# Kernel optimization log

Hardware: AMD Instinct MI355X
Metric: run time of the kernel (lower is better)

The kernel has to match this reference:

```python
import jax, jax.numpy as jnp
import numpy as np


def setup_inputs() -> dict:
    key = jax.random.key(0)
    ks = jax.random.split(key, 8)
    N, T, U = 8, 200, 50
    E = D = J = 512
    V = 500
    s = lambda k, shape, fan_in: jax.random.normal(k, shape, jnp.float32) / np.sqrt(fan_in)
    return {
        "encoder_out": jax.random.normal(ks[0], (N, T, E), jnp.float32),
        "decoder_out": jax.random.normal(ks[1], (N, U, D), jnp.float32),
        "W_enc": s(ks[2], (J, E), E),
        "b_enc": jax.random.normal(ks[3], (J,), jnp.float32) * 0.01,
        "W_dec": s(ks[4], (J, D), D),
        "b_dec": jax.random.normal(ks[5], (J,), jnp.float32) * 0.01,
        "W_out": s(ks[6], (V, J), J),
        "b_out": jax.random.normal(ks[7], (V,), jnp.float32) * 0.01,
    }


def reference(encoder_out, decoder_out, W_enc, b_enc, W_dec, b_dec, W_out, b_out):
    # Project encoder (N,T,E)->(N,T,J) and decoder (N,U,D)->(N,U,J).
    enc_p = jnp.einsum("nte,je->ntj", encoder_out, W_enc) + b_enc
    dec_p = jnp.einsum("nud,jd->nuj", decoder_out, W_dec) + b_dec
    # Broadcast add -> (N,T,U,J), tanh, then linear to vocab -> (N,T,U,V).
    activations = jnp.tanh(enc_p[:, :, None, :] + dec_p[:, None, :, :])
    logits = jnp.einsum("ntuj,vj->ntuv", activations, W_out) + b_out
    return logits
```

## Files before the change

### kernel.cpp

```cpp
#include <hip/hip_runtime.h>
#include <hip/hip_bf16.h>
#include <stdint.h>

#define JD 512
#define VV 500

typedef short short8 __attribute__((ext_vector_type(8)));
typedef short short4v __attribute__((ext_vector_type(4)));
typedef float floatx4 __attribute__((ext_vector_type(4)));

__device__ inline short f2bf(float f) {
    uint32_t u = __float_as_uint(f);
    uint32_t r = (u + 0x7FFFu + ((u >> 16) & 1u)) >> 16;
    return (short)r;
}

__device__ inline float fast_tanh(float x) {
    float e = __builtin_amdgcn_exp2f(x * 2.8853900817779268f);
    return 1.0f - 2.0f * __builtin_amdgcn_rcpf(e + 1.0f);
}

__global__ __launch_bounds__(256) void prep_kernel(
    const float* __restrict__ Wout, short* __restrict__ WbF)
{
    int j = blockIdx.x * 256 + threadIdx.x;
    int l16 = j & 15;
    int q4  = (j >> 4) & 3;
    int in  = (j >> 6) & 7;
    int wn  = (j >> 9) & 3;
    int ks  = j >> 11;
    int v  = wn * 128 + in * 16 + l16;
    int k0 = ks * 32 + q4 * 8;
    short8 o;
    if (v < VV) {
        const float4* p = (const float4*)(Wout + (size_t)v * JD + k0);
        float4 a = p[0], b = p[1];
        o[0] = f2bf(a.x); o[1] = f2bf(a.y); o[2] = f2bf(a.z); o[3] = f2bf(a.w);
        o[4] = f2bf(b.x); o[5] = f2bf(b.y); o[6] = f2bf(b.z); o[7] = f2bf(b.w);
    } else {
        o = (short8){0,0,0,0,0,0,0,0};
    }
    *(short8*)(WbF + (size_t)j * 8) = o;
}

#define PST 72
__global__ __launch_bounds__(256) void proj_gemm(
    const float* __restrict__ enc, const float* __restrict__ dec,
    const float* __restrict__ Wenc, const float* __restrict__ Wdec,
    const float* __restrict__ b_enc, const float* __restrict__ b_dec,
    float* __restrict__ enc_p, float* __restrict__ dec_p)
{
    __shared__ short As[64 * PST];
    __shared__ short Bs[64 * PST];
    int bx = blockIdx.x, by = blockIdx.y;
    const float* A; const float* W; const float* bias; float* C; int M;
    if (bx < 25) { A = enc; W = Wenc; bias = b_enc; C = enc_p; M = 1600; }
    else { bx -= 25; A = dec; W = Wdec; bias = b_dec; C = dec_p; M = 400; }

    int tid = threadIdx.x;
    int lane = tid & 63, wv = tid >> 6;
    int wm = wv >> 1, wn = wv & 1;
    int l16 = lane & 15, q4 = lane >> 4;

    int ra = tid >> 2, ha = tid & 3;
    int m_st = bx * 64 + ra;
    bool valid = m_st < M;
    int wrow = by * 64 + ra;

    floatx4 acc[2][2];
    #pragma unroll
    for (int a = 0; a < 2; a++)
        #pragma unroll
        for (int b = 0; b < 2; b++) acc[a][b] = (floatx4){0.f, 0.f, 0.f, 0.f};

    for (int kk = 0; kk < 8; kk++) {
        int k0 = kk * 64;
        __syncthreads();
        {
            float4 v0 = make_float4(0.f, 0.f, 0.f, 0.f);
            float4 v1 = v0, v2 = v0, v3 = v0;
            if (valid) {
                const float4* p = (const float4*)(A + (size_t)m_st * JD + k0 + ha * 16);
                v0 = p[0]; v1 = p[1]; v2 = p[2]; v3 = p[3];
            }
            short8 o0, o1;
            o0[0] = f2bf(v0.x); o0[1] = f2bf(v0.y); o0[2] = f2bf(v0.z); o0[3] = f2bf(v0.w);
            o0[4] = f2bf(v1.x); o0[5] = f2bf(v1.y); o0[6] = f2bf(v1.z); o0[7] = f2bf(v1.w);
            o1[0] = f2bf(v2.x); o1[1] = f2bf(v2.y); o1[2] = f2bf(v2.z); o1[3] = f2bf(v2.w);
            o1[4] = f2bf(v3.x); o1[5] = f2bf(v3.y); o1[6] = f2bf(v3.z); o1[7] = f2bf(v3.w);
            *(short8*)&As[ra * PST + ha * 16]     = o0;
            *(short8*)&As[ra * PST + ha * 16 + 8] = o1;

            const float4* pb = (const float4*)(W + (size_t)wrow * JD + k0 + ha * 16);
            float4 w0 = pb[0], w1 = pb[1], w2 = pb[2], w3 = pb[3];
            short8 p0, p1;
            p0[0] = f2bf(w0.x); p0[1] = f2bf(w0.y); p0[2] = f2bf(w0.z); p0[3] = f2bf(w0.w);
            p0[4] = f2bf(w1.x); p0[5] = f2bf(w1.y); p0[6] = f2bf(w1.z); p0[7] = f2bf(w1.w);
            p1[0] = f2bf(w2.x); p1[1] = f2bf(w2.y); p1[2] = f2bf(w2.z); p1[3] = f2bf(w2.w);
            p1[4] = f2bf(w3.x); p1[5] = f2bf(w3.y); p1[6] = f2bf(w3.z); p1[7] = f2bf(w3.w);
            *(short8*)&Bs[ra * PST + ha * 16]     = p0;
            *(short8*)&Bs[ra * PST + ha * 16 + 8] = p1;
        }
        __syncthreads();
        #pragma unroll
        for (int h2 = 0; h2 < 2; h2++) {
            short8 af[2], bf[2];
            #pragma unroll
            for (int im = 0; im < 2; im++)
                af[im] = *(const short8*)&As[(wm * 32 + im * 16 + l16) * PST + h2 * 32 + q4 * 8];
            #pragma unroll
            for (int in = 0; in < 2; in++)
                bf[in] = *(const short8*)&Bs[(wn * 32 + in * 16 + l16) * PST + h2 * 32 + q4 * 8];
            #pragma unroll
            for (int im = 0; im < 2; im++)
                #pragma unroll
                for (int in = 0; in < 2; in++)
                    acc[im][in] = __builtin_amdgcn_mfma_f32_16x16x32_bf16(
                        af[im], bf[in], acc[im][in], 0, 0, 0);
        }
    }
    #pragma unroll
    for (int im = 0; im < 2; im++) {
        int mb = bx * 64 + wm * 32 + im * 16 + q4 * 4;
        #pragma unroll
        for (int rr = 0; rr < 4; rr++) {
            int m = mb + rr;
            if (m < M) {
                #pragma unroll
                for (int in = 0; in < 2; in++) {
                    int j = by * 64 + wn * 32 + in * 16 + l16;
                    C[(size_t)m * JD + j] = acc[im][in][rr] + bias[j];
                }
            }
        }
    }
}

#define AST 520
__global__ __launch_bounds__(512, 2) void fused_joiner(
    const float* __restrict__ enc_p, const float* __restrict__ dec_p,
    const short* __restrict__ WbF, const float* __restrict__ b_out,
    float* __restrict__ out)
{
    __shared__ short As[2][64 * AST];
    int tid = threadIdx.x;
    int mgrp = blockIdx.x;
    int vg   = blockIdx.y;
    int lane = tid & 63, wv = tid >> 6;
    int l16 = lane & 15, q4 = lane >> 4;

    int wn  = vg * 2 + (wv >> 2);
    int in0 = (wv & 3) * 2;
    int vb0 = wn * 128 + in0 * 16;

    short8 breg0[16], breg1[16];
    {
        const short* bp = WbF + q4 * 128 + l16 * 8 + (wn * 8 + in0) * 512;
        #pragma unroll
        for (int ks = 0; ks < 16; ks++) {
            breg0[ks] = *(const short8*)(bp + ks * 16384);
            breg1[ks] = *(const short8*)(bp + ks * 16384 + 512);
        }
    }

    float bo0, bo1;
    {
        int v0 = vb0 + l16, v1 = vb0 + 16 + l16;
        bo0 = (v0 < VV) ? b_out[v0] : 0.f;
        bo1 = (v1 < VV) ? b_out[v1] : 0.f;
    }

    int rsub = tid >> 7;
    int jf   = (tid & 127) * 4;

    for (int t = 0; t < 10; t++) {
        int m0 = (mgrp * 10 + t) * 64;
        short* buf = &As[t & 1][0];

        #pragma unroll 4
        for (int pass = 0; pass < 16; pass++) {
            int row = pass * 4 + rsub;
            int m = m0 + row;
            int er = m / 50;
            int n  = m / 10000;
            int dr = n * 50 + (m - er * 50);
            float4 e = *(const float4*)(enc_p + (size_t)er * JD + jf);
            float4 d = *(const float4*)(dec_p + (size_t)dr * JD + jf);
            short4v o;
            o[0] = f2bf(fast_tanh(e.x + d.x));
            o[1] = f2bf(fast_tanh(e.y + d.y));
            o[2] = f2bf(fast_tanh(e.z + d.z));
            o[3] = f2bf(fast_tanh(e.w + d.w));
            *(short4v*)&buf[row * AST + jf] = o;
        }
        __syncthreads();

        #pragma unroll
        for (int ms = 0; ms < 4; ms++) {
            int ab = (ms * 16 + l16) * AST + q4 * 8;
            floatx4 a0 = (floatx4){0.f, 0.f, 0.f, 0.f};
            floatx4 a1 = (floatx4){0.f, 0.f, 0.f, 0.f};
            #pragma unroll
            for (int ks = 0; ks < 16; ks++) {
                short8 af = *(const short8*)&buf[ab + ks * 32];
                a0 = __builtin_amdgcn_mfma_f32_16x16x32_bf16(af, breg0[ks], a0, 0, 0, 0);
                a1 = __builtin_amdgcn_mfma_f32_16x16x32_bf16(af, breg1[ks], a1, 0, 0, 0);
            }
            int v0 = vb0 + l16, v1 = vb0 + 16 + l16;
            #pragma unroll
            for (int rr = 0; rr < 4; rr++) {
                size_t orow = (size_t)(m0 + ms * 16 + q4 * 4 + rr) * VV;
                if (v0 < VV) out[orow + v0] = a0[rr] + bo0;
                if (v1 < VV) out[orow + v1] = a1[rr] + bo1;
            }
        }
    }
}

extern "C" void kernel_launch(void* const* d_in, const int* in_sizes, int n_in,
                              void* d_out, int out_size, void* d_ws, size_t ws_size,
                              hipStream_t stream)
{
    const float* enc   = (const float*)d_in[0];
    const float* dec   = (const float*)d_in[1];
    const float* Wenc  = (const float*)d_in[2];
    const float* b_enc = (const float*)d_in[3];
    const float* Wdec  = (const float*)d_in[4];
    const float* b_dec = (const float*)d_in[5];
    const float* Wout  = (const float*)d_in[6];
    const float* b_out = (const float*)d_in[7];
    float* out = (float*)d_out;

    char* ws = (char*)d_ws;
    short* WbF   = (short*)(ws + 0);
    float* enc_p = (float*)(ws + 524288);
    float* dec_p = (float*)(ws + 3801088);

    prep_kernel<<<128, 256, 0, stream>>>(Wout, WbF);
    proj_gemm<<<dim3(32, 8), 256, 0, stream>>>(enc, dec, Wenc, Wdec,
                                               b_enc, b_dec, enc_p, dec_p);
    fused_joiner<<<dim3(125, 2), 512, 0, stream>>>(enc_p, dec_p, WbF, b_out, out);
}
```

Before: 238.3 us.

## Software-pipeline tanh tile generation with MFMA and load full K in projection

The main joint kernel now builds the first activation tile up front. While the MFMAs run on the current tile, it prefetches enc/dec rows and writes the tanh'd bf16 values for the next tile into the other LDS buffer, so the tanh/load phase overlaps with matrix work. The projection GEMM now stages the whole K=512 extent of A and W into LDS in one pass, with one barrier instead of a per-chunk loop with two barriers. That raises LDS use to about 133KB per block, which may cut occupancy or exceed the LDS limit, and the prefetch adds register pressure.

Result: no change. 234.0 us (-1.8%).

```diff
diff --git a/kernel.cpp b/kernel.cpp
--- a/kernel.cpp
+++ b/kernel.cpp
@@ -43,15 +43,15 @@
     *(short8*)(WbF + (size_t)j * 8) = o;
 }
 
-#define PST 72
+#define QST 520
 __global__ __launch_bounds__(256) void proj_gemm(
     const float* __restrict__ enc, const float* __restrict__ dec,
     const float* __restrict__ Wenc, const float* __restrict__ Wdec,
     const float* __restrict__ b_enc, const float* __restrict__ b_dec,
     float* __restrict__ enc_p, float* __restrict__ dec_p)
 {
-    __shared__ short As[64 * PST];
-    __shared__ short Bs[64 * PST];
+    __shared__ short As[64 * QST];
+    __shared__ short Bs[64 * QST];
     int bx = blockIdx.x, by = blockIdx.y;
     const float* A; const float* W; const float* bias; float* C; int M;
     if (bx < 25) { A = enc; W = Wenc; bias = b_enc; C = enc_p; M = 1600; }
@@ -67,58 +67,57 @@
     bool valid = m_st < M;
     int wrow = by * 64 + ra;
 
+    #pragma unroll
+    for (int c = 0; c < 8; c++) {
+        int k0 = c * 64 + ha * 16;
+        float4 v0 = make_float4(0.f, 0.f, 0.f, 0.f);
+        float4 v1 = v0, v2 = v0, v3 = v0;
+        if (valid) {
+            const float4* p = (const float4*)(A + (size_t)m_st * JD + k0);
+            v0 = p[0]; v1 = p[1]; v2 = p[2]; v3 = p[3];
+        }
+        const float4* pb = (const float4*)(W + (size_t)wrow * JD + k0);
+        float4 w0 = pb[0], w1 = pb[1], w2 = pb[2], w3 = pb[3];
+        short8 o0, o1, p0, p1;
+        o0[0] = f2bf(v0.x); o0[1] = f2bf(v0.y); o0[2] = f2bf(v0.z); o0[3] = f2bf(v0.w);
+        o0[4] = f2bf(v1.x); o0[5] = f2bf(v1.y); o0[6] = f2bf(v1.z); o0[7] = f2bf(v1.w);
+        o1[0] = f2bf(v2.x); o1[1] = f2bf(v2.y); o1[2] = f2bf(v2.z); o1[3] = f2bf(v2.w);
+        o1[4] = f2bf(v3.x); o1[5] = f2bf(v3.y); o1[6] = f2bf(v3.z); o1[7] = f2bf(v3.w);
+        p0[0] = f2bf(w0.x); p0[1] = f2bf(w0.y); p0[2] = f2bf(w0.z); p0[3] = f2bf(w0.w);
+        p0[4] = f2bf(w1.x); p0[5] = f2bf(w1.y); p0[6] = f2bf(w1.z); p0[7] = f2bf(w1.w);
+        p1[0] = f2bf(w2.x); p1[1] = f2bf(w2.y); p1[2] = f2bf(w2.z); p1[3] = f2bf(w2.w);
+        p1[4] = f2bf(w3.x); p1[5] = f2bf(w3.y); p1[6] = f2bf(w3.z); p1[7] = f2bf(w3.w);
+        *(short8*)&As[ra * QST + k0]     = o0;
+        *(short8*)&As[ra * QST + k0 + 8] = o1;
+        *(short8*)&Bs[ra * QST + k0]     = p0;
+        *(short8*)&Bs[ra * QST + k0 + 8] = p1;
+    }
+    __syncthreads();
+
     floatx4 acc[2][2];
     #pragma unroll
     for (int a = 0; a < 2; a++)
         #pragma unroll
         for (int b = 0; b < 2; b++) acc[a][b] = (floatx4){0.f, 0.f, 0.f, 0.f};
 
-    for (int kk = 0; kk < 8; kk++) {
-        int k0 = kk * 64;
-        __syncthreads();
-        {
-            float4 v0 = make_float4(0.f, 0.f, 0.f, 0.f);
-            float4 v1 = v0, v2 = v0, v3 = v0;
-            if (valid) {
-                const float4* p = (const float4*)(A + (size_t)m_st * JD + k0 + ha * 16);
-                v0 = p[0]; v1 = p[1]; v2 = p[2]; v3 = p[3];
-            }
-            short8 o0, o1;
-            o0[0] = f2bf(v0.x); o0[1] = f2bf(v0.y); o0[2] = f2bf(v0.z); o0[3] = f2bf(v0.w);
-            o0[4] = f2bf(v1.x); o0[5] = f2bf(v1.y); o0[6] = f2bf(v1.z); o0[7] = f2bf(v1.w);
-            o1[0] = f2bf(v2.x); o1[1] = f2bf(v2.y); o1[2] = f2bf(v2.z); o1[3] = f2bf(v2.w);
-            o1[4] = f2bf(v3.x); o1[5] = f2bf(v3.y); o1[6] = f2bf(v3.z); o1[7] = f2bf(v3.w);
-            *(short8*)&As[ra * PST + ha * 16]     = o0;
-            *(short8*)&As[ra * PST + ha * 16 + 8] = o1;
-
-            const float4* pb = (const float4*)(W + (size_t)wrow * JD + k0 + ha * 16);
-            float4 w0 = pb[0], w1 = pb[1], w2 = pb[2], w3 = pb[3];
-            short8 p0, p1;
-            p0[0] = f2bf(w0.x); p0[1] = f2bf(w0.y); p0[2] = f2bf(w0.z); p0[3] = f2bf(w0.w);
-            p0[4] = f2bf(w1.x); p0[5] = f2bf(w1.y); p0[6] = f2bf(w1.z); p0[7] = f2bf(w1.w);
-            p1[0] = f2bf(w2.x); p1[1] = f2bf(w2.y); p1[2] = f2bf(w2.z); p1[3] = f2bf(w2.w);
-            p1[4] = f2bf(w3.x); p1[5] = f2bf(w3.y); p1[6] = f2bf(w3.z); p1[7] = f2bf(w3.w);
-            *(short8*)&Bs[ra * PST + ha * 16]     = p0;
-            *(short8*)&Bs[ra * PST + ha * 16 + 8] = p1;
-        }
-        __syncthreads();
-        #pragma unroll
-        for (int h2 = 0; h2 < 2; h2++) {
-            short8 af[2], bf[2];
-            #pragma unroll
-            for (int im = 0; im < 2; im++)
-                af[im] = *(const short8*)&As[(wm * 32 + im * 16 + l16) * PST + h2 * 32 + q4 * 8];
+    #pragma unroll
+    for (int ks = 0; ks < 16; ks++) {
+        int ko = ks * 32 + q4 * 8;
+        short8 af[2], bf[2];
+        #pragma unroll
+        for (int im = 0; im < 2; im++)
+            af[im] = *(const short8*)&As[(wm * 32 + im * 16 + l16) * QST + ko];
+        #pragma unroll
+        for (int in = 0; in < 2; in++)
+            bf[in] = *(const short8*)&Bs[(wn * 32 + in * 16 + l16) * QST + ko];
+        #pragma unroll
+        for (int im = 0; im < 2; im++)
             #pragma unroll
             for (int in = 0; in < 2; in++)
-                bf[in] = *(const short8*)&Bs[(wn * 32 + in * 16 + l16) * PST + h2 * 32 + q4 * 8];
-            #pragma unroll
-            for (int im = 0; im < 2; im++)
-                #pragma unroll
-                for (int in = 0; in < 2; in++)
-                    acc[im][in] = __builtin_amdgcn_mfma_f32_16x16x32_bf16(
-                        af[im], bf[in], acc[im][in], 0, 0, 0);
-        }
-    }
+                acc[im][in] = __builtin_amdgcn_mfma_f32_16x16x32_bf16(
+                    af[im], bf[in], acc[im][in], 0, 0, 0);
+    }
+
     #pragma unroll
     for (int im = 0; im < 2; im++) {
         int mb = bx * 64 + wm * 32 + im * 16 + q4 * 4;
@@ -173,10 +172,8 @@
     int rsub = tid >> 7;
     int jf   = (tid & 127) * 4;
 
-    for (int t = 0; t < 10; t++) {
-        int m0 = (mgrp * 10 + t) * 64;
-        short* buf = &As[t & 1][0];
-
+    {
+        int m0 = mgrp * 640;
         #pragma unroll 4
         for (int pass = 0; pass < 16; pass++) {
             int row = pass * 4 + rsub;
@@ -191,12 +188,36 @@
             o[1] = f2bf(fast_tanh(e.y + d.y));
             o[2] = f2bf(fast_tanh(e.z + d.z));
             o[3] = f2bf(fast_tanh(e.w + d.w));
-            *(short4v*)&buf[row * AST + jf] = o;
-        }
-        __syncthreads();
+            *(short4v*)&As[0][row * AST + jf] = o;
+        }
+    }
+    __syncthreads();
+
+    for (int t = 0; t < 10; t++) {
+        int m0 = (mgrp * 10 + t) * 64;
+        const short* buf = &As[t & 1][0];
+        short* nbuf = &As[(t + 1) & 1][0];
+        int m0n = m0 + 64;
+        bool pf = (t < 9);
 
         #pragma unroll
         for (int ms = 0; ms < 4; ms++) {
+            float4 pe[4], pd[4];
+            int prow[4];
+            if (pf) {
+                #pragma unroll
+                for (int p = 0; p < 4; p++) {
+                    int row = ms * 16 + p * 4 + rsub;
+                    int m = m0n + row;
+                    int er = m / 50;
+                    int n  = m / 10000;
+                    int dr = n * 50 + (m - er * 50);
+                    prow[p] = row;
+                    pe[p] = *(const float4*)(enc_p + (size_t)er * JD + jf);
+                    pd[p] = *(const float4*)(dec_p + (size_t)dr * JD + jf);
+                }
+            }
+
             int ab = (ms * 16 + l16) * AST + q4 * 8;
             floatx4 a0 = (floatx4){0.f, 0.f, 0.f, 0.f};
             floatx4 a1 = (floatx4){0.f, 0.f, 0.f, 0.f};
@@ -206,6 +227,19 @@
                 a0 = __builtin_amdgcn_mfma_f32_16x16x32_bf16(af, breg0[ks], a0, 0, 0, 0);
                 a1 = __builtin_amdgcn_mfma_f32_16x16x32_bf16(af, breg1[ks], a1, 0, 0, 0);
             }
+
+            if (pf) {
+                #pragma unroll
+                for (int p = 0; p < 4; p++) {
+                    short4v o;
+                    o[0] = f2bf(fast_tanh(pe[p].x + pd[p].x));
+                    o[1] = f2bf(fast_tanh(pe[p].y + pd[p].y));
+                    o[2] = f2bf(fast_tanh(pe[p].z + pd[p].z));
+                    o[3] = f2bf(fast_tanh(pe[p].w + pd[p].w));
+                    *(short4v*)&nbuf[prow[p] * AST + jf] = o;
+                }
+            }
+
             int v0 = vb0 + l16, v1 = vb0 + 16 + l16;
             #pragma unroll
             for (int rr = 0; rr < 4; rr++) {
@@ -214,6 +248,7 @@
                 if (v1 < VV) out[orow + v1] = a1[rr] + bo1;
             }
         }
+        __syncthreads();
     }
 }
 
```
